# Kernel tuning notes

Hardware: AMD Instinct MI355X
Metric: run time of the kernel (lower is better)

Reference implementation:

```python
import jax, jax.numpy as jnp
import numpy as np
from jax import lax

H = 24  # hidden_states
FORGET_BIAS = 1.0  # TF LSTMCell default


def setup_inputs() -> dict:
    key = jax.random.key(0)
    ks = jax.random.split(key, 10)
    B, T, V, E, C = 256, 512, 50000, 200, 3
    return {
        "words": jax.random.randint(ks[0], (B, T), 0, V, dtype=jnp.int32),
        "capitals": jax.random.randint(ks[1], (B, T), 0, C, dtype=jnp.int32),
        "Ew": jax.random.normal(ks[2], (V, E), dtype=jnp.float32),
        "Ec": jax.random.normal(ks[3], (C, C), dtype=jnp.float32),
        "W_lstm": jax.random.normal(ks[4], (E + C + H, 4 * H), dtype=jnp.float32) * 0.1,
        "b_lstm": jnp.zeros((4 * H,), dtype=jnp.float32),
        "W1": jax.random.normal(ks[5], (H, 50), dtype=jnp.float32) * 0.2,
        "b1": jnp.full((50,), 0.1, dtype=jnp.float32),
        "W2": jax.random.normal(ks[6], (50, 6), dtype=jnp.float32) * 0.2,
        "b2": jnp.zeros((6,), dtype=jnp.float32),
    }


def reference(words, capitals, Ew, Ec, W_lstm, b_lstm, W1, b1, W2, b2):
    # embed + concat: [B, T, 203]
    x = jnp.concatenate([Ew[words], Ec[capitals]], axis=-1)
    B = x.shape[0]
    xs = jnp.swapaxes(x, 0, 1)  # [T, B, F]

    def step(carry, xt):
        c, h = carry
        z = jnp.concatenate([xt, h], axis=-1) @ W_lstm + b_lstm  # [B, 4H]
        i, j, f, o = jnp.split(z, 4, axis=-1)  # TF gate order i, j, f, o
        c = jax.nn.sigmoid(f + FORGET_BIAS) * c + jax.nn.sigmoid(i) * jnp.tanh(j)
        h = jax.nn.sigmoid(o) * jnp.tanh(c)
        return (c, h), h

    init = (jnp.zeros((B, H), x.dtype), jnp.zeros((B, H), x.dtype))
    _, hs = lax.scan(step, init, xs)  # hs: [T, B, H]

    last = hs.mean(axis=0)                       # mean-pool over time: [B, H]
    layer = jax.nn.elu(last @ W1 + b1)           # [B, 50]
    return jax.nn.sigmoid(layer @ W2 + b2)       # [B, 6]
```

## Files before the change

kernel.cpp:

```cpp
#include <hip/hip_runtime.h>

typedef float f2 __attribute__((ext_vector_type(2)));

constexpr int Tt = 512;
constexpr int Bb = 256;
constexpr int Ee = 200;
constexpr int Gg = 96;
constexpr int Vv = 50000;

__device__ __forceinline__ float fast_rcp(float x) { return __builtin_amdgcn_rcpf(x); }
__device__ __forceinline__ float sigf(float x) { return fast_rcp(1.f + __expf(-x)); }
__device__ __forceinline__ float tanhf_(float x) {
    float e = __expf(2.f * x);
    return 1.f - 2.f * fast_rcp(e + 1.f);
}

__global__ __launch_bounds__(256) void ew_proj(const float* __restrict__ Ew,
                                               const float* __restrict__ Wl,
                                               float* __restrict__ EwW)
{
    __shared__ float As[8][64];
    __shared__ float Bs[8][96];
    const int tid = threadIdx.x;
    const int w0  = blockIdx.x * 64;
    const int tr  = tid >> 4;
    const int tc  = tid & 15;
    const int am  = tid >> 2;
    const int ak  = (tid & 3) * 2;
    const int bk  = tid >> 5;
    const int bg  = (tid & 31) * 3;

    const int wA = w0 + am;
    const float* aptr = Ew + (long)((wA < Vv) ? wA : (Vv - 1)) * Ee + ak;
    const float* bptr = Wl + bk * Gg + bg;
    int gp[3];
    #pragma unroll
    for (int u = 0; u < 3; ++u) { const int g = bg + u; gp[u] = (g % 24) * 4 + g / 24; }

    f2    avr  = *(const f2*)(aptr);
    float bvr0 = bptr[0], bvr1 = bptr[1], bvr2 = bptr[2];

    f2 acc[4][3] = {};

    for (int k0 = 0; k0 < Ee; k0 += 8) {
        As[ak][am]     = avr.x;
        As[ak + 1][am] = avr.y;
        Bs[bk][gp[0]] = bvr0; Bs[bk][gp[1]] = bvr1; Bs[bk][gp[2]] = bvr2;
        __syncthreads();

        if (k0 + 8 < Ee) {
            avr  = *(const f2*)(aptr + k0 + 8);
            const long bo = (long)(k0 + 8) * Gg;
            bvr0 = bptr[bo + 0]; bvr1 = bptr[bo + 1]; bvr2 = bptr[bo + 2];
        }

        #pragma unroll
        for (int kk = 0; kk < 8; ++kk) {
            const float4 a4 = *(const float4*)&As[kk][tr * 4];
            f2 b[3];
            #pragma unroll
            for (int u = 0; u < 3; ++u) b[u] = *(const f2*)&Bs[kk][tc * 6 + u * 2];
            #pragma unroll
            for (int i = 0; i < 4; ++i) {
                const float ai = (&a4.x)[i];
                f2 a2 = {ai, ai};
                #pragma unroll
                for (int u = 0; u < 3; ++u) acc[i][u] += a2 * b[u];
            }
        }
        __syncthreads();
    }
    #pragma unroll
    for (int i = 0; i < 4; ++i) {
        const int w = w0 + tr * 4 + i;
        if (w < Vv) {
            #pragma unroll
            for (int u = 0; u < 3; ++u)
                *(f2*)(EwW + (long)w * Gg + tc * 6 + u * 2) = acc[i][u];
        }
    }
}

#define REP24(M) M(0)M(1)M(2)M(3)M(4)M(5)M(6)M(7)M(8)M(9)M(10)M(11) \
                 M(12)M(13)M(14)M(15)M(16)M(17)M(18)M(19)M(20)M(21)M(22)M(23)

__global__ __launch_bounds__(64, 1) void lstm_head(
    const int* __restrict__ words, const int* __restrict__ caps,
    const float* __restrict__ Ec,  const float* __restrict__ Wl,
    const float* __restrict__ bl,  const float* __restrict__ EwW,
    const float* __restrict__ W1,  const float* __restrict__ b1,
    const float* __restrict__ W2,  const float* __restrict__ b2,
    float* __restrict__ out)
{
    __shared__ float4 EcB[3][24];
    __shared__ float  hmean[2][24];
    __shared__ float  a1buf[2][50];

    const int  lane = threadIdx.x;
    const int  half = lane >> 5;
    const int  j    = lane & 31;
    const int  jc   = (j < 24) ? j : 23;
    const bool act  = (j < 24);
    const int  b    = blockIdx.x * 2 + half;

    for (int e = lane; e < 72; e += 64) {
        const int cap = e / 24, jj = e % 24;
        float4 v;
        #pragma unroll
        for (int c = 0; c < 4; ++c) {
            float s = bl[c * 24 + jj];
            #pragma unroll
            for (int kk = 0; kk < 3; ++kk)
                s += Ec[cap * 3 + kk] * Wl[(200 + kk) * Gg + c * 24 + jj];
            (&v.x)[c] = s;
        }
        EcB[cap][jj] = v;
    }
    __syncthreads();

#define DECL_U(K) f2 uij##K, ufo##K;
    REP24(DECL_U)
#undef DECL_U
#define LOAD_U(K) { const int base_ = (203 + K) * Gg + jc;      \
                    uij##K.x = Wl[base_ +  0];                  \
                    uij##K.y = Wl[base_ + 24];                  \
                    ufo##K.x = Wl[base_ + 48];                  \
                    ufo##K.y = Wl[base_ + 72]; }
    REP24(LOAD_U)
#undef LOAD_U
#define PIN_U(K) asm volatile("" : "+v"(uij##K), "+v"(ufo##K));
    REP24(PIN_U)
#undef PIN_U

    const int* wrow = words + b * Tt;
    const int* crow = caps  + b * Tt;
    const int  off  = jc * 4;

    float4 x0 = *(const float4*)(EwW + (long)wrow[0] * Gg + off);
    float4 x1 = *(const float4*)(EwW + (long)wrow[1] * Gg + off);
    float4 x2 = *(const float4*)(EwW + (long)wrow[2] * Gg + off);
    int wi3 = wrow[3], wi4 = wrow[4];
    int cp0 = crow[0], cp1 = crow[1], cp2 = crow[2], cp3 = crow[3], cp4 = crow[4];

    float4 ecb = EcB[cp0][jc];
    float cstate = 0.f, hsum = 0.f, hn = 0.f;

    for (int t = 0; t < Tt; ++t) {
        const float4 x3 = *(const float4*)(EwW + (long)wi3 * Gg + off);
        const int tn  = (t + 5 < Tt) ? (t + 5) : (Tt - 1);
        const int win = wrow[tn];
        const int cpn = crow[tn];

        f2 zij_a, zfo_a, zij_b = {0.f, 0.f}, zfo_b = {0.f, 0.f};
        zij_a.x = x0.x + ecb.x;  zij_a.y = x0.y + ecb.y;
        zfo_a.x = x0.z + ecb.z;  zfo_a.y = x0.w + ecb.w;

        const int hu = __float_as_int(hn);
#define STEP_A(K) { const float hk_ = __int_as_float(                          \
                        __builtin_amdgcn_ds_swizzle(hu, ((K) << 5)));          \
                    f2 h2_ = {hk_, hk_};                                       \
                    zij_a += h2_ * uij##K;  zfo_a += h2_ * ufo##K; }
#define STEP_B(K) { const float hk_ = __int_as_float(                          \
                        __builtin_amdgcn_ds_swizzle(hu, ((K) << 5)));          \
                    f2 h2_ = {hk_, hk_};                                       \
                    zij_b += h2_ * uij##K;  zfo_b += h2_ * ufo##K; }
        STEP_A(0)  STEP_A(1)  STEP_A(2)  STEP_A(3)  STEP_A(4)  STEP_A(5)
        STEP_A(6)  STEP_A(7)  STEP_A(8)  STEP_A(9)  STEP_A(10) STEP_A(11)
        STEP_B(12) STEP_B(13) STEP_B(14) STEP_B(15) STEP_B(16) STEP_B(17)
        STEP_B(18) STEP_B(19) STEP_B(20) STEP_B(21) STEP_B(22) STEP_B(23)
#undef STEP_A
#undef STEP_B

        const f2 zij = zij_a + zij_b;
        const f2 zfo = zfo_a + zfo_b;

        const float ig = sigf(zij.x);
        const float tj = tanhf_(zij.y);
        const float fg = sigf(zfo.x + 1.0f);
        const float og = sigf(zfo.y);
        cstate = fg * cstate + ig * tj;
        hn = og * tanhf_(cstate);
        hsum += hn;

        ecb = EcB[cp1][jc];
        x0 = x1; x1 = x2; x2 = x3;
        wi3 = wi4; wi4 = win;
        cp0 = cp1; cp1 = cp2; cp2 = cp3; cp3 = cp4; cp4 = cpn;
    }

    if (act) hmean[half][jc] = hsum * (1.f / (float)Tt);
    __syncthreads();

    if (j < 25) {
        #pragma unroll
        for (int p = 0; p < 2; ++p) {
            const int q = j + p * 25;
            float s = b1[q];
            #pragma unroll
            for (int k = 0; k < 24; ++k)
                s += hmean[half][k] * W1[k * 50 + q];
            a1buf[half][q] = (s > 0.f) ? s : (__expf(s) - 1.f);
        }
    }
    __syncthreads();

    if (j < 6) {
        float s = b2[j];
        for (int q = 0; q < 50; ++q) s += a1buf[half][q] * W2[q * 6 + j];
        out[b * 6 + j] = sigf(s);
    }
}

extern "C" void kernel_launch(void* const* d_in, const int* in_sizes, int n_in,
                              void* d_out, int out_size, void* d_ws, size_t ws_size,
                              hipStream_t stream)
{
    const int*   words = (const int*)d_in[0];
    const int*   caps  = (const int*)d_in[1];
    const float* Ew    = (const float*)d_in[2];
    const float* Ec    = (const float*)d_in[3];
    const float* Wl    = (const float*)d_in[4];
    const float* bl    = (const float*)d_in[5];
    const float* W1    = (const float*)d_in[6];
    const float* b1    = (const float*)d_in[7];
    const float* W2    = (const float*)d_in[8];
    const float* b2    = (const float*)d_in[9];
    float* out = (float*)d_out;
    float* EwW = (float*)d_ws;

    ew_proj<<<(Vv + 63) / 64, 256, 0, stream>>>(Ew, Wl, EwW);
    lstm_head<<<Bb / 2, 64, 0, stream>>>(words, caps, Ec, Wl, bl, EwW,
                                         W1, b1, W2, b2, out);
}
```

Measured before the change: 406.6 us.

## Assign one batch row per wave and broadcast hidden state via readlane

```diff
diff --git a/kernel.cpp b/kernel.cpp
--- a/kernel.cpp
+++ b/kernel.cpp
@@ -93,15 +93,12 @@
     float* __restrict__ out)
 {
     __shared__ float4 EcB[3][24];
-    __shared__ float  hmean[2][24];
-    __shared__ float  a1buf[2][50];
-
-    const int  lane = threadIdx.x;
-    const int  half = lane >> 5;
-    const int  j    = lane & 31;
-    const int  jc   = (j < 24) ? j : 23;
-    const bool act  = (j < 24);
-    const int  b    = blockIdx.x * 2 + half;
+    __shared__ float  hmean[24];
+    __shared__ float  a1buf[50];
+
+    const int lane = threadIdx.x;
+    const int u    = (lane < 24) ? lane : 23;
+    const int b    = blockIdx.x;
 
     for (int e = lane; e < 72; e += 64) {
         const int cap = e / 24, jj = e % 24;
@@ -118,23 +115,18 @@
     }
     __syncthreads();
 
-#define DECL_U(K) f2 uij##K, ufo##K;
-    REP24(DECL_U)
-#undef DECL_U
-#define LOAD_U(K) { const int base_ = (203 + K) * Gg + jc;      \
-                    uij##K.x = Wl[base_ +  0];                  \
-                    uij##K.y = Wl[base_ + 24];                  \
-                    ufo##K.x = Wl[base_ + 48];                  \
-                    ufo##K.y = Wl[base_ + 72]; }
-    REP24(LOAD_U)
-#undef LOAD_U
-#define PIN_U(K) asm volatile("" : "+v"(uij##K), "+v"(ufo##K));
-    REP24(PIN_U)
-#undef PIN_U
+#define DECL_UK(K) float ui##K, uj##K, uf##K, uo##K;
+    REP24(DECL_UK)
+#undef DECL_UK
+#define LOAD_UK(K) { const float* p_ = Wl + (203 + K) * Gg + u;  \
+                     ui##K = p_[0];  uj##K = p_[24];             \
+                     uf##K = p_[48]; uo##K = p_[72]; }
+    REP24(LOAD_UK)
+#undef LOAD_UK
 
     const int* wrow = words + b * Tt;
     const int* crow = caps  + b * Tt;
-    const int  off  = jc * 4;
+    const int  off  = u * 4;
 
     float4 x0 = *(const float4*)(EwW + (long)wrow[0] * Gg + off);
     float4 x1 = *(const float4*)(EwW + (long)wrow[1] * Gg + off);
@@ -142,8 +134,8 @@
     int wi3 = wrow[3], wi4 = wrow[4];
     int cp0 = crow[0], cp1 = crow[1], cp2 = crow[2], cp3 = crow[3], cp4 = crow[4];
 
-    float4 ecb = EcB[cp0][jc];
-    float cstate = 0.f, hsum = 0.f, hn = 0.f;
+    float4 ecb = EcB[cp0][u];
+    float cst = 0.f, hsum = 0.f, hn = 0.f;
 
     for (int t = 0; t < Tt; ++t) {
         const float4 x3 = *(const float4*)(EwW + (long)wi3 * Gg + off);
@@ -151,63 +143,74 @@
         const int win = wrow[tn];
         const int cpn = crow[tn];
 
-        f2 zij_a, zfo_a, zij_b = {0.f, 0.f}, zfo_b = {0.f, 0.f};
-        zij_a.x = x0.x + ecb.x;  zij_a.y = x0.y + ecb.y;
-        zfo_a.x = x0.z + ecb.z;  zfo_a.y = x0.w + ecb.w;
-
-        const int hu = __float_as_int(hn);
-#define STEP_A(K) { const float hk_ = __int_as_float(                          \
-                        __builtin_amdgcn_ds_swizzle(hu, ((K) << 5)));          \
-                    f2 h2_ = {hk_, hk_};                                       \
-                    zij_a += h2_ * uij##K;  zfo_a += h2_ * ufo##K; }
-#define STEP_B(K) { const float hk_ = __int_as_float(                          \
-                        __builtin_amdgcn_ds_swizzle(hu, ((K) << 5)));          \
-                    f2 h2_ = {hk_, hk_};                                       \
-                    zij_b += h2_ * uij##K;  zfo_b += h2_ * ufo##K; }
-        STEP_A(0)  STEP_A(1)  STEP_A(2)  STEP_A(3)  STEP_A(4)  STEP_A(5)
-        STEP_A(6)  STEP_A(7)  STEP_A(8)  STEP_A(9)  STEP_A(10) STEP_A(11)
-        STEP_B(12) STEP_B(13) STEP_B(14) STEP_B(15) STEP_B(16) STEP_B(17)
-        STEP_B(18) STEP_B(19) STEP_B(20) STEP_B(21) STEP_B(22) STEP_B(23)
-#undef STEP_A
-#undef STEP_B
-
-        const f2 zij = zij_a + zij_b;
-        const f2 zfo = zfo_a + zfo_b;
-
-        const float ig = sigf(zij.x);
-        const float tj = tanhf_(zij.y);
-        const float fg = sigf(zfo.x + 1.0f);
-        const float og = sigf(zfo.y);
-        cstate = fg * cstate + ig * tj;
-        hn = og * tanhf_(cstate);
+        asm volatile("" :: "v"(ui0),"v"(uj0),"v"(uf0),"v"(uo0),
+                           "v"(ui1),"v"(uj1),"v"(uf1),"v"(uo1),
+                           "v"(ui2),"v"(uj2),"v"(uf2),"v"(uo2));
+        asm volatile("" :: "v"(ui3),"v"(uj3),"v"(uf3),"v"(uo3),
+                           "v"(ui4),"v"(uj4),"v"(uf4),"v"(uo4),
+                           "v"(ui5),"v"(uj5),"v"(uf5),"v"(uo5));
+        asm volatile("" :: "v"(ui6),"v"(uj6),"v"(uf6),"v"(uo6),
+                           "v"(ui7),"v"(uj7),"v"(uf7),"v"(uo7),
+                           "v"(ui8),"v"(uj8),"v"(uf8),"v"(uo8));
+        asm volatile("" :: "v"(ui9),"v"(uj9),"v"(uf9),"v"(uo9),
+                           "v"(ui10),"v"(uj10),"v"(uf10),"v"(uo10),
+                           "v"(ui11),"v"(uj11),"v"(uf11),"v"(uo11));
+        asm volatile("" :: "v"(ui12),"v"(uj12),"v"(uf12),"v"(uo12),
+                           "v"(ui13),"v"(uj13),"v"(uf13),"v"(uo13),
+                           "v"(ui14),"v"(uj14),"v"(uf14),"v"(uo14));
+        asm volatile("" :: "v"(ui15),"v"(uj15),"v"(uf15),"v"(uo15),
+                           "v"(ui16),"v"(uj16),"v"(uf16),"v"(uo16),
+                           "v"(ui17),"v"(uj17),"v"(uf17),"v"(uo17));
+        asm volatile("" :: "v"(ui18),"v"(uj18),"v"(uf18),"v"(uo18),
+                           "v"(ui19),"v"(uj19),"v"(uf19),"v"(uo19),
+                           "v"(ui20),"v"(uj20),"v"(uf20),"v"(uo20));
+        asm volatile("" :: "v"(ui21),"v"(uj21),"v"(uf21),"v"(uo21),
+                           "v"(ui22),"v"(uj22),"v"(uf22),"v"(uo22),
+                           "v"(ui23),"v"(uj23),"v"(uf23),"v"(uo23));
+
+        float zi = x0.x + ecb.x;
+        float zj = x0.y + ecb.y;
+        float zf = x0.z + ecb.z;
+        float zo = x0.w + ecb.w;
+
+        const int hni = __float_as_int(hn);
+#define KSTEP(K) { const float hk_ = __int_as_float(                     \
+                       __builtin_amdgcn_readlane(hni, K));               \
+                   zi += hk_ * ui##K;  zj += hk_ * uj##K;                \
+                   zf += hk_ * uf##K;  zo += hk_ * uo##K; }
+        REP24(KSTEP)
+#undef KSTEP
+
+        const float ig = sigf(zi);
+        const float tj = tanhf_(zj);
+        const float fg = sigf(zf + 1.0f);
+        const float og = sigf(zo);
+        cst = fg * cst + ig * tj;
+        hn  = og * tanhf_(cst);
         hsum += hn;
 
-        ecb = EcB[cp1][jc];
+        ecb = EcB[cp1][u];
         x0 = x1; x1 = x2; x2 = x3;
         wi3 = wi4; wi4 = win;
         cp0 = cp1; cp1 = cp2; cp2 = cp3; cp3 = cp4; cp4 = cpn;
     }
 
-    if (act) hmean[half][jc] = hsum * (1.f / (float)Tt);
+    if (lane < 24) hmean[lane] = hsum * (1.f / (float)Tt);
     __syncthreads();
 
-    if (j < 25) {
+    if (lane < 50) {
+        float s = b1[lane];
         #pragma unroll
-        for (int p = 0; p < 2; ++p) {
-            const int q = j + p * 25;
-            float s = b1[q];
-            #pragma unroll
-            for (int k = 0; k < 24; ++k)
-                s += hmean[half][k] * W1[k * 50 + q];
-            a1buf[half][q] = (s > 0.f) ? s : (__expf(s) - 1.f);
-        }
+        for (int k = 0; k < 24; ++k)
+            s += hmean[k] * W1[k * 50 + lane];
+        a1buf[lane] = (s > 0.f) ? s : (__expf(s) - 1.f);
     }
     __syncthreads();
 
-    if (j < 6) {
-        float s = b2[j];
-        for (int q = 0; q < 50; ++q) s += a1buf[half][q] * W2[q * 6 + j];
-        out[b * 6 + j] = sigf(s);
+    if (lane < 6) {
+        float s = b2[lane];
+        for (int q = 0; q < 50; ++q) s += a1buf[q] * W2[q * 6 + lane];
+        out[b * 6 + lane] = sigf(s);
     }
 }
 
@@ -229,6 +232,6 @@
     float* EwW = (float*)d_ws;
 
     ew_proj<<<(Vv + 63) / 64, 256, 0, stream>>>(Ew, Wl, EwW);
-    lstm_head<<<Bb / 2, 64, 0, stream>>>(words, caps, Ec, Wl, bl, EwW,
-                                         W1, b1, W2, b2, out);
-}
+    lstm_head<<<Bb, 64, 0, stream>>>(words, caps, Ec, Wl, bl, EwW,
+                                     W1, b1, W2, b2, out);
+}
```

New measurement: 377.8 us. -7.1%, faster.
